# Kernel tuning notes

Hardware: AMD Instinct MI355X
Metric: run time of the kernel (lower is better)

The kernel has to match this reference:

```python
import jax, jax.numpy as jnp
import numpy as np

HIDDEN_NF = 256
ATOMICA_DIM = 512
NUM_HEADS = 4
HEAD_DIM = HIDDEN_NF // NUM_HEADS
EDGE_CUTOFF = 10.0
N_LIG = 1024
N_POCKET = 8192
BOX = 30.0  # Angstrom box so the cutoff mask is selective


def _lin(key, fan_in, fan_out):
    kw, kb = jax.random.split(key)
    s = 1.0 / np.sqrt(fan_in)
    W = jax.random.uniform(kw, (fan_in, fan_out), jnp.float32, -s, s)
    b = jax.random.uniform(kb, (fan_out,), jnp.float32, -s, s)
    return W, b


def setup_inputs() -> dict:
    key = jax.random.key(0)
    ks = jax.random.split(key, 12)
    h_lig = jax.random.normal(ks[0], (N_LIG, HIDDEN_NF), jnp.float32)
    x_lig = jax.random.uniform(ks[1], (N_LIG, 3), jnp.float32) * BOX
    h_atomica = jax.random.normal(ks[2], (N_POCKET, ATOMICA_DIM), jnp.float32)
    x_pocket = jax.random.uniform(ks[3], (N_POCKET, 3), jnp.float32) * BOX
    qw, qb = _lin(ks[4], HIDDEN_NF, HIDDEN_NF)
    kw, kb = _lin(ks[5], ATOMICA_DIM, HIDDEN_NF)
    vw, vb = _lin(ks[6], ATOMICA_DIM, HIDDEN_NF)
    ow, ob = _lin(ks[7], HIDDEN_NF, HIDDEN_NF)
    e1w, e1b = _lin(ks[8], 1, HIDDEN_NF)
    e2w, e2b = _lin(ks[9], HIDDEN_NF, NUM_HEADS)
    c1w, c1b = _lin(ks[10], HIDDEN_NF, HIDDEN_NF)
    c2w, c2b = _lin(ks[11], HIDDEN_NF, 1)
    return dict(h_lig=h_lig, x_lig=x_lig, h_atomica=h_atomica, x_pocket=x_pocket,
                qw=qw, qb=qb, kw=kw, kb=kb, vw=vw, vb=vb, ow=ow, ob=ob,
                e1w=e1w, e1b=e1b, e2w=e2w, e2b=e2b,
                c1w=c1w, c1b=c1b, c2w=c2w, c2b=c2b)


def reference(h_lig, x_lig, h_atomica, x_pocket,
              qw, qb, kw, kb, vw, vb, ow, ob,
              e1w, e1b, e2w, e2b, c1w, c1b, c2w, c2b):
    N_lig = h_lig.shape[0]
    silu = jax.nn.silu
    # pairwise geometry: [N_lig, N_pocket, 3]
    rel_pos = x_pocket[None, :, :] - x_lig[:, None, :]
    distances = jnp.linalg.norm(rel_pos, axis=-1, keepdims=True)  # [Nl,Np,1]
    # edge bias MLP: [Nl,Np,num_heads]
    edge_attr = silu(distances @ e1w + e1b) @ e2w + e2b
    mask = distances[..., 0] < EDGE_CUTOFF  # [Nl,Np]
    Q = (h_lig @ qw + qb).reshape(N_lig, NUM_HEADS, HEAD_DIM)
    K = (h_atomica @ kw + kb).reshape(-1, NUM_HEADS, HEAD_DIM)
    V = (h_atomica @ vw + vb).reshape(-1, NUM_HEADS, HEAD_DIM)
    scores = jnp.einsum('ihd,jhd->ijh', Q, K) / np.sqrt(HEAD_DIM).astype(np.float32)
    scores = scores + edge_attr
    scores = jnp.where(mask[..., None], scores, -jnp.inf)
    attn = jax.nn.softmax(scores, axis=1)
    attn = jnp.where(jnp.isnan(attn), 0.0, attn)  # nan_to_num for fully-masked rows
    h_attended = jnp.einsum('ijh,jhd->ihd', attn, V).reshape(N_lig, HIDDEN_NF)
    h_out = h_lig + h_attended @ ow + ob
    # equivariant coordinate update
    normalized_rel_pos = rel_pos / (distances + 1e-8)
    avg_attn = attn.mean(axis=-1, keepdims=True)  # [Nl,Np,1]
    coord_messages = (avg_attn * normalized_rel_pos).sum(axis=1)  # [Nl,3]
    coord_scale = silu(h_attended @ c1w + c1b) @ c2w + c2b  # [Nl,1]
    x_out = x_lig + coord_scale * coord_messages
    return h_out, x_out
```

## Files before the change

kernel.cpp:

```cpp
#include <hip/hip_runtime.h>
#include <hip/hip_bf16.h>


#define NLIG   1024
#define NPOCK  8192
#define HIDDEN 256
#define ADIM   512
#define NHEAD  4
#define HDIM   64
#define NTAB   1024
#define NSPLIT 32
#define CHUNK  (NPOCK / NSPLIT)
#define LOG2E  1.4426950408889634f
#define QK_SCALE (0.125f * LOG2E)

typedef float f32x16 __attribute__((ext_vector_type(16)));
typedef short short8 __attribute__((ext_vector_type(8)));

union U4S8 { uint4 u; short8 s; };

static __device__ __forceinline__ float exp2h(float x) {
  float r; asm("v_exp_f32 %0, %1" : "=v"(r) : "v"(x)); return r;
}
static __device__ __forceinline__ float rsqh(float x) {
  float r; asm("v_rsq_f32 %0, %1" : "=v"(r) : "v"(x)); return r;
}
static __device__ __forceinline__ unsigned cvtpk(float lo, float hi) {
  unsigned r;
  asm("v_cvt_pk_bf16_f32 %0, %1, %2" : "=v"(r) : "v"(lo), "v"(hi));
  return r;
}
static __device__ __forceinline__ unsigned short f2bf(float f) {
  union { __hip_bfloat16 h; unsigned short u; } c;
  c.h = __float2bfloat16(f);
  return c.u;
}
static __device__ __forceinline__ float bf2f(unsigned u16) {
  union { unsigned uu; float f; } c;
  c.uu = u16 << 16;
  return c.f;
}
static __device__ __forceinline__ short8 load_bf8(const unsigned short* p) {
  U4S8 t; t.u = *(const uint4*)p; return t.s;
}
static __device__ __forceinline__ f32x16 mfma32(short8 a, short8 b, f32x16 c) {
  return __builtin_amdgcn_mfma_f32_32x32x16_bf16(a, b, c, 0, 0, 0);
}

#define NCAST 4352
#define NTRANS 448
__global__ __launch_bounds__(256)
void prep_kernel(const float* __restrict__ hA, const float* __restrict__ hl,
                 const float* __restrict__ qw, const float* __restrict__ kw,
                 const float* __restrict__ vw, const float* __restrict__ ow,
                 const float* __restrict__ c1w,
                 const float* __restrict__ e1w, const float* __restrict__ e1b,
                 const float* __restrict__ e2w, const float* __restrict__ e2b,
                 unsigned short* __restrict__ hAb, unsigned short* __restrict__ hlb,
                 unsigned short* __restrict__ qwT, unsigned short* __restrict__ kwT,
                 unsigned short* __restrict__ vwT, unsigned short* __restrict__ owT,
                 unsigned short* __restrict__ c1wT, float* __restrict__ tabG) {
  int bx = blockIdx.x;
  int tid = threadIdx.x;
  if (bx < NCAST) {
    int id = bx * 256 + tid;
    const int nA4 = NPOCK * ADIM / 4;
    if (id < nA4) {
      float4 v = ((const float4*)hA)[id];
      ushort4 o; o.x = f2bf(v.x); o.y = f2bf(v.y); o.z = f2bf(v.z); o.w = f2bf(v.w);
      ((ushort4*)hAb)[id] = o;
    } else {
      int j = id - nA4;
      float4 v = ((const float4*)hl)[j];
      ushort4 o; o.x = f2bf(v.x); o.y = f2bf(v.y); o.z = f2bf(v.z); o.w = f2bf(v.w);
      ((ushort4*)hlb)[j] = o;
    }
  } else if (bx < NCAST + NTRANS) {
    int b = bx - NCAST;
    const float* src; unsigned short* dst; int K;
    if (b < 64)       { src = qw;  dst = qwT;  K = 256; }
    else if (b < 192) { src = kw;  dst = kwT;  K = 512; b -= 64; }
    else if (b < 320) { src = vw;  dst = vwT;  K = 512; b -= 192; }
    else if (b < 384) { src = ow;  dst = owT;  K = 256; b -= 320; }
    else              { src = c1w; dst = c1wT; K = 256; b -= 384; }
    int kt = K / 32;
    int k0 = (b % kt) * 32, n0 = (b / kt) * 32;
    __shared__ float tile[32][33];
    int tx = tid & 31, ty = tid >> 5;
#pragma unroll
    for (int r = 0; r < 4; ++r)
      tile[ty + 8 * r][tx] = src[(k0 + ty + 8 * r) * 256 + n0 + tx];
    __syncthreads();
#pragma unroll
    for (int r = 0; r < 4; ++r)
      dst[(n0 + ty + 8 * r) * K + k0 + tx] = f2bf(tile[tx][ty + 8 * r]);
  } else {
    int eb = bx - (NCAST + NTRANS);
    int w = tid >> 6, l = tid & 63;
    int entry = eb * 4 + w;
    float d = (entry + 0.5f) * (10.0f / NTAB);
    float a0 = 0.f, a1 = 0.f, a2 = 0.f, a3 = 0.f;
#pragma unroll
    for (int jj = 0; jj < 4; ++jj) {
      int j = l + jj * 64;
      float v = fmaf(d, e1w[j], e1b[j]);
      float s = v / (1.0f + __expf(-v));
      float4 w2 = ((const float4*)e2w)[j];
      a0 = fmaf(s, w2.x, a0);
      a1 = fmaf(s, w2.y, a1);
      a2 = fmaf(s, w2.z, a2);
      a3 = fmaf(s, w2.w, a3);
    }
#pragma unroll
    for (int m = 32; m >= 1; m >>= 1) {
      a0 += __shfl_xor(a0, m); a1 += __shfl_xor(a1, m);
      a2 += __shfl_xor(a2, m); a3 += __shfl_xor(a3, m);
    }
    if (l == 0) {
      tabG[0 * NTAB + entry] = (a0 + e2b[0]) * LOG2E;
      tabG[1 * NTAB + entry] = (a1 + e2b[1]) * LOG2E;
      tabG[2 * NTAB + entry] = (a2 + e2b[2]) * LOG2E;
      tabG[3 * NTAB + entry] = (a3 + e2b[3]) * LOG2E;
    }
  }
}

__global__ __launch_bounds__(256)
void kv_gemm_kernel(const unsigned short* __restrict__ hAb,
                    const unsigned short* __restrict__ kwT, const unsigned short* __restrict__ vwT,
                    const float* __restrict__ kb, const float* __restrict__ vb,
                    unsigned short* __restrict__ Kb, unsigned short* __restrict__ VTb) {
  int tid = threadIdx.x;
  int w = tid >> 6, lane = tid & 63;
  int lo = lane & 31, hi = lane >> 5;
  int m0 = blockIdx.x * 128 + w * 32;
  int n0 = blockIdx.y * 32;
  const unsigned short* ap  = hAb + (size_t)(m0 + lo) * ADIM + hi * 8;
  const unsigned short* bkp = kwT + (size_t)(n0 + lo) * ADIM + hi * 8;
  const unsigned short* bvp = vwT + (size_t)(n0 + lo) * ADIM + hi * 8;
  f32x16 aK, aV;
#pragma unroll
  for (int i = 0; i < 16; ++i) { aK[i] = 0.f; aV[i] = 0.f; }
#pragma unroll 8
  for (int kk = 0; kk < ADIM / 16; ++kk) {
    short8 a  = load_bf8(ap + kk * 16);
    short8 bk = load_bf8(bkp + kk * 16);
    short8 bv = load_bf8(bvp + kk * 16);
    aK = mfma32(a, bk, aK);
    aV = mfma32(bv, a, aV);
  }
  int n = n0 + lo;
  float bnK = kb[n];
#pragma unroll
  for (int g = 0; g < 4; ++g) {
#pragma unroll
    for (int rr = 0; rr < 4; ++rr) {
      int r = g * 4 + rr;
      int row = g * 8 + hi * 4 + rr;
      Kb[(size_t)(m0 + row) * HIDDEN + n] = f2bf(aK[r] + bnK);
      int nv = n0 + row;
      VTb[(size_t)nv * NPOCK + m0 + lo] = f2bf(aV[r] + vb[nv]);
    }
  }
}

template <int MODE>
__global__ __launch_bounds__(64)
void gemm32_kernel(const unsigned short* __restrict__ A, const unsigned short* __restrict__ BT,
                   const float* __restrict__ bias, void* __restrict__ out,
                   const float* __restrict__ resid, int M, int N, int K) {
  int lane = threadIdx.x;
  int lo = lane & 31, hi = lane >> 5;
  int m0 = blockIdx.x * 32, n0 = blockIdx.y * 32;
  const unsigned short* ap = A + (size_t)(m0 + lo) * K + hi * 8;
  const unsigned short* bp = BT + (size_t)(n0 + lo) * K + hi * 8;
  f32x16 acc;
#pragma unroll
  for (int i = 0; i < 16; ++i) acc[i] = 0.f;
  int nk = K / 16;
#pragma unroll 4
  for (int kk = 0; kk < nk; ++kk) {
    short8 a = load_bf8(ap + kk * 16);
    short8 b = load_bf8(bp + kk * 16);
    acc = mfma32(a, b, acc);
  }
  int n = n0 + lo;
  float bn = bias[n];
#pragma unroll
  for (int g = 0; g < 4; ++g) {
#pragma unroll
    for (int rr = 0; rr < 4; ++rr) {
      int r = g * 4 + rr;
      int m = m0 + g * 8 + hi * 4 + rr;
      float v = acc[r] + bn;
      if (MODE == 0) {
        ((unsigned short*)out)[(size_t)m * N + n] = f2bf(v);
      } else if (MODE == 2) {
        ((float*)out)[(size_t)m * N + n] = v + resid[(size_t)m * N + n];
      } else {
        float sg = v / (1.0f + exp2h(-LOG2E * v));
        ((unsigned short*)out)[(size_t)m * N + n] = f2bf(sg);
      }
    }
  }
}

__global__ __launch_bounds__(256)
void attn_kernel(const unsigned short* __restrict__ Qbf, const unsigned short* __restrict__ Kbf,
                 const unsigned short* __restrict__ VTbf,
                 const float* __restrict__ x_lig, const float* __restrict__ x_pocket,
                 const float* __restrict__ tabG,
                 unsigned* __restrict__ partOb, float4* __restrict__ partZC) {
  __shared__ float4 xch[CHUNK];
  __shared__ float tab[NHEAD][NTAB];

  int tid = threadIdx.x;
  int h = tid >> 6;
  int lane = tid & 63;
  int lo = lane & 31, hi = lane >> 5;
  int qt = blockIdx.x & 31;
  int split = blockIdx.x >> 5;
  int q0 = qt * 32;
  int j0g = split * CHUNK;

  for (int i = tid; i < CHUNK; i += 256) {
    float x = x_pocket[(j0g + i) * 3 + 0];
    float y = x_pocket[(j0g + i) * 3 + 1];
    float z = x_pocket[(j0g + i) * 3 + 2];
    float4 v; v.x = x; v.y = y; v.z = z; v.w = 0.f;
    xch[i] = v;
  }
  for (int i = tid; i < NHEAD * NTAB; i += 256) ((float*)tab)[i] = tabG[i];
  __syncthreads();

  int q = q0 + lo;
  float xl0 = x_lig[q * 3 + 0];
  float xl1 = x_lig[q * 3 + 1];
  float xl2 = x_lig[q * 3 + 2];

  short8 qfr[4];
#pragma unroll
  for (int kk = 0; kk < 4; ++kk)
    qfr[kk] = load_bf8(Qbf + (size_t)q * HIDDEN + h * HDIM + kk * 16 + hi * 8);

  f32x16 O0, O1;
#pragma unroll
  for (int i = 0; i < 16; ++i) { O0[i] = 0.f; O1[i] = 0.f; }
  float Z = 0.f, c0 = 0.f, c1 = 0.f, c2 = 0.f;

#pragma unroll 1
  for (int t = 0; t < CHUNK / 32; ++t) {
    int jb = t * 32;
    f32x16 s;
#pragma unroll
    for (int i = 0; i < 16; ++i) s[i] = 0.f;
#pragma unroll
    for (int kk = 0; kk < 4; ++kk) {
      short8 a = load_bf8(Kbf + (size_t)(j0g + jb + lo) * HIDDEN + h * HDIM + kk * 16 + hi * 8);
      s = mfma32(a, qfr[kk], s);
    }
    unsigned wp[8];
    float pprev = 0.f;
#pragma unroll
    for (int r = 0; r < 16; ++r) {
      int jl = (r & 3) + 8 * (r >> 2) + 4 * hi;
      float4 xp = xch[jb + jl];
      float dx = xp.x - xl0, dy = xp.y - xl1, dz = xp.z - xl2;
      float r2 = fmaf(dx, dx, fmaf(dy, dy, dz * dz));
      float r2c = fmaxf(r2, 1e-24f);
      float rinv = rsqh(r2c);
      float d = r2c * rinv;
      int idx = (int)(d * (NTAB / 10.0f));
      idx = idx > (NTAB - 1) ? (NTAB - 1) : idx;
      float b = tab[h][idx];
      float s2 = fmaf(s[r], QK_SCALE, b);
      float pe = (r2 < 100.0f) ? exp2h(s2) : 0.0f;
      Z += pe;
      float pr = pe * rinv;
      c0 = fmaf(pr, dx, c0);
      c1 = fmaf(pr, dy, c1);
      c2 = fmaf(pr, dz, c2);
      if (r & 1) wp[r >> 1] = cvtpk(pprev, pe); else pprev = pe;
    }
#pragma unroll
    for (int sub = 0; sub < 2; ++sub) {
      unsigned W0 = wp[sub * 4 + 0], W1 = wp[sub * 4 + 1];
      unsigned W2 = wp[sub * 4 + 2], W3 = wp[sub * 4 + 3];
      unsigned e01 = (unsigned)__shfl_xor((int)(hi ? W0 : W2), 32);
      unsigned e23 = (unsigned)__shfl_xor((int)(hi ? W1 : W3), 32);
      U4S8 pb;
      pb.u.x = hi ? e01 : W0;
      pb.u.y = hi ? e23 : W1;
      pb.u.z = hi ? W2 : e01;
      pb.u.w = hi ? W3 : e23;
      const unsigned short* vbase =
          VTbf + (size_t)(h * HDIM + lo) * NPOCK + j0g + jb + sub * 16 + hi * 8;
      short8 v0 = load_bf8(vbase);
      short8 v1 = load_bf8(vbase + (size_t)32 * NPOCK);
      O0 = mfma32(v0, pb.s, O0);
      O1 = mfma32(v1, pb.s, O1);
    }
  }

  unsigned* po = partOb + (size_t)(((q * NHEAD) + h) * NSPLIT + split) * (HDIM / 2);
#pragma unroll
  for (int g = 0; g < 4; ++g) {
    uint2 u0;
    u0.x = cvtpk(O0[g * 4 + 0], O0[g * 4 + 1]);
    u0.y = cvtpk(O0[g * 4 + 2], O0[g * 4 + 3]);
    *(uint2*)(po + (g * 8 + hi * 4) / 2) = u0;
    uint2 u1;
    u1.x = cvtpk(O1[g * 4 + 0], O1[g * 4 + 1]);
    u1.y = cvtpk(O1[g * 4 + 2], O1[g * 4 + 3]);
    *(uint2*)(po + (32 + g * 8 + hi * 4) / 2) = u1;
  }
  float Zt = Z + __shfl_xor(Z, 32);
  float c0t = c0 + __shfl_xor(c0, 32);
  float c1t = c1 + __shfl_xor(c1, 32);
  float c2t = c2 + __shfl_xor(c2, 32);
  if (hi == 0) {
    float4 zc; zc.x = Zt; zc.y = c0t; zc.z = c1t; zc.w = c2t;
    partZC[((q * NHEAD) + h) * NSPLIT + split] = zc;
  }
}

__global__ __launch_bounds__(256)
void combine_kernel(const unsigned short* __restrict__ partOb, const float4* __restrict__ partZC,
                    unsigned short* __restrict__ hattb, float* __restrict__ cmsg) {
  int q = blockIdx.x;
  int t = threadIdx.x;
  int h = t >> 6, dl = t & 63;
  float Zh = 0.f;
#pragma unroll
  for (int s = 0; s < NSPLIT; ++s) Zh += partZC[(q * NHEAD + h) * NSPLIT + s].x;
  float o = 0.f;
#pragma unroll
  for (int s = 0; s < NSPLIT; ++s)
    o += bf2f(partOb[(size_t)((q * NHEAD + h) * NSPLIT + s) * HDIM + dl]);
  float inv = (Zh > 0.f) ? 1.0f / Zh : 0.f;
  hattb[(size_t)q * HIDDEN + h * HDIM + dl] = f2bf(o * inv);

  __shared__ float sm[NHEAD][3];
  if (t < NHEAD) {
    float zz = 0.f, a0 = 0.f, a1 = 0.f, a2 = 0.f;
    for (int s = 0; s < NSPLIT; ++s) {
      float4 v = partZC[(q * NHEAD + t) * NSPLIT + s];
      zz += v.x; a0 += v.y; a1 += v.z; a2 += v.w;
    }
    float iv = (zz > 0.f) ? 0.25f / zz : 0.f;
    sm[t][0] = a0 * iv; sm[t][1] = a1 * iv; sm[t][2] = a2 * iv;
  }
  __syncthreads();
  if (t < 3) cmsg[q * 3 + t] = sm[0][t] + sm[1][t] + sm[2][t] + sm[3][t];
}

__global__ __launch_bounds__(64)
void coord_kernel(const unsigned short* __restrict__ c1out, const float* __restrict__ c2w,
                  const float* __restrict__ c2b, const float* __restrict__ cmsg,
                  const float* __restrict__ x_lig, float* __restrict__ x_out) {
  int q = blockIdx.x;
  int lane = threadIdx.x;
  const unsigned short* row = c1out + (size_t)q * HIDDEN + lane * 4;
  ushort4 tv = *(const ushort4*)row;
  float4 wv = *(const float4*)(c2w + lane * 4);
  float acc = bf2f(tv.x) * wv.x + bf2f(tv.y) * wv.y + bf2f(tv.z) * wv.z + bf2f(tv.w) * wv.w;
#pragma unroll
  for (int m = 32; m >= 1; m >>= 1) acc += __shfl_xor(acc, m);
  if (lane == 0) {
    float sc = acc + c2b[0];
    x_out[q * 3 + 0] = x_lig[q * 3 + 0] + sc * cmsg[q * 3 + 0];
    x_out[q * 3 + 1] = x_lig[q * 3 + 1] + sc * cmsg[q * 3 + 1];
    x_out[q * 3 + 2] = x_lig[q * 3 + 2] + sc * cmsg[q * 3 + 2];
  }
}

extern "C" void kernel_launch(void* const* d_in, const int* in_sizes, int n_in,
                              void* d_out, int out_size, void* d_ws, size_t ws_size,
                              hipStream_t stream) {
  const float* h_lig  = (const float*)d_in[0];
  const float* x_lig  = (const float*)d_in[1];
  const float* h_atom = (const float*)d_in[2];
  const float* x_pock = (const float*)d_in[3];
  const float* qw  = (const float*)d_in[4];
  const float* qb  = (const float*)d_in[5];
  const float* kw  = (const float*)d_in[6];
  const float* kb  = (const float*)d_in[7];
  const float* vw  = (const float*)d_in[8];
  const float* vb  = (const float*)d_in[9];
  const float* ow  = (const float*)d_in[10];
  const float* ob  = (const float*)d_in[11];
  const float* e1w = (const float*)d_in[12];
  const float* e1b = (const float*)d_in[13];
  const float* e2w = (const float*)d_in[14];
  const float* e2b = (const float*)d_in[15];
  const float* c1w = (const float*)d_in[16];
  const float* c1b = (const float*)d_in[17];
  const float* c2w = (const float*)d_in[18];
  const float* c2b = (const float*)d_in[19];

  char* w = (char*)d_ws;
  unsigned short* hAb  = (unsigned short*)w; w += (size_t)NPOCK * ADIM * 2;
  unsigned short* hlb  = (unsigned short*)w; w += (size_t)NLIG * HIDDEN * 2;
  unsigned short* qwT  = (unsigned short*)w; w += 256 * 256 * 2;
  unsigned short* kwT  = (unsigned short*)w; w += 256 * 512 * 2;
  unsigned short* vwT  = (unsigned short*)w; w += 256 * 512 * 2;
  unsigned short* owT  = (unsigned short*)w; w += 256 * 256 * 2;
  unsigned short* c1wT = (unsigned short*)w; w += 256 * 256 * 2;
  unsigned short* Qb   = (unsigned short*)w; w += (size_t)NLIG * HIDDEN * 2;
  unsigned short* Kb   = (unsigned short*)w; w += (size_t)NPOCK * HIDDEN * 2;
  unsigned short* VTb  = (unsigned short*)w; w += (size_t)HIDDEN * NPOCK * 2;
  float* tabG          = (float*)w;          w += NHEAD * NTAB * 4;
  unsigned* partOb     = (unsigned*)w;       w += (size_t)NLIG * NHEAD * NSPLIT * HDIM * 2;
  float* partZC        = (float*)w;          w += (size_t)NLIG * NHEAD * NSPLIT * 4 * 4;
  unsigned short* hatt = (unsigned short*)w; w += (size_t)NLIG * HIDDEN * 2;
  unsigned short* c1o  = (unsigned short*)w; w += (size_t)NLIG * HIDDEN * 2;
  float* cmsg          = (float*)w;          w += (size_t)NLIG * 3 * 4;

  float* hout = (float*)d_out;
  float* xout = ((float*)d_out) + (size_t)NLIG * HIDDEN;

  prep_kernel<<<NCAST + NTRANS + NTAB / 4, 256, 0, stream>>>(
      h_atom, h_lig, qw, kw, vw, ow, c1w, e1w, e1b, e2w, e2b,
      hAb, hlb, qwT, kwT, vwT, owT, c1wT, tabG);
  kv_gemm_kernel<<<dim3(NPOCK / 128, HIDDEN / 32), 256, 0, stream>>>(
      hAb, kwT, vwT, kb, vb, Kb, VTb);
  gemm32_kernel<0><<<dim3(NLIG / 32, HIDDEN / 32), 64, 0, stream>>>(
      hlb, qwT, qb, (void*)Qb, nullptr, NLIG, HIDDEN, HIDDEN);
  attn_kernel<<<32 * NSPLIT, 256, 0, stream>>>(Qb, Kb, VTb, x_lig, x_pock, tabG,
                                               partOb, (float4*)partZC);
  combine_kernel<<<NLIG, 256, 0, stream>>>((const unsigned short*)partOb,
                                           (const float4*)partZC, hatt, cmsg);
  gemm32_kernel<2><<<dim3(NLIG / 32, HIDDEN / 32), 64, 0, stream>>>(
      hatt, owT, ob, (void*)hout, h_lig, NLIG, HIDDEN, HIDDEN);
  gemm32_kernel<3><<<dim3(NLIG / 32, HIDDEN / 32), 64, 0, stream>>>(
      hatt, c1wT, c1b, (void*)c1o, nullptr, NLIG, HIDDEN, HIDDEN);
  coord_kernel<<<NLIG, 64, 0, stream>>>(c1o, c2w, c2b, cmsg, x_lig, xout);
}
```

Before: 208.7 us.

## Fuse Q/KV projections and output epilogue GEMMs, prefetch K/V in attention, halve splits

Merges the Q projection into the K/V projection kernel and merges the output projection, the coord MLP GEMM and the c2 dot product into one epilogue kernel that uses atomics to accumulate the coordinate scale. The attention loop now prefetches the next K tile and the current V tiles before the MFMAs to hide load latency, and the sequence split count drops from 32 to 16. The aim is fewer launches and better latency hiding, at the cost of less attention-grid parallelism, an extra memset, and atomic accumulation order that makes the coordinate scale nondeterministic.

```diff
diff --git a/kernel.cpp b/kernel.cpp
--- a/kernel.cpp
+++ b/kernel.cpp
@@ -9,8 +9,9 @@
 #define NHEAD  4
 #define HDIM   64
 #define NTAB   1024
-#define NSPLIT 32
+#define NSPLIT 16
 #define CHUNK  (NPOCK / NSPLIT)
+#define NT     (CHUNK / 32)
 #define LOG2E  1.4426950408889634f
 #define QK_SCALE (0.125f * LOG2E)
 
@@ -126,80 +127,67 @@
 }
 
 __global__ __launch_bounds__(256)
-void kv_gemm_kernel(const unsigned short* __restrict__ hAb,
-                    const unsigned short* __restrict__ kwT, const unsigned short* __restrict__ vwT,
-                    const float* __restrict__ kb, const float* __restrict__ vb,
-                    unsigned short* __restrict__ Kb, unsigned short* __restrict__ VTb) {
+void proj_kernel(const unsigned short* __restrict__ hAb, const unsigned short* __restrict__ hlb,
+                 const unsigned short* __restrict__ kwT, const unsigned short* __restrict__ vwT,
+                 const unsigned short* __restrict__ qwT,
+                 const float* __restrict__ kb, const float* __restrict__ vb,
+                 const float* __restrict__ qb,
+                 unsigned short* __restrict__ Kb, unsigned short* __restrict__ VTb,
+                 unsigned short* __restrict__ Qb) {
   int tid = threadIdx.x;
   int w = tid >> 6, lane = tid & 63;
   int lo = lane & 31, hi = lane >> 5;
-  int m0 = blockIdx.x * 128 + w * 32;
   int n0 = blockIdx.y * 32;
-  const unsigned short* ap  = hAb + (size_t)(m0 + lo) * ADIM + hi * 8;
-  const unsigned short* bkp = kwT + (size_t)(n0 + lo) * ADIM + hi * 8;
-  const unsigned short* bvp = vwT + (size_t)(n0 + lo) * ADIM + hi * 8;
-  f32x16 aK, aV;
-#pragma unroll
-  for (int i = 0; i < 16; ++i) { aK[i] = 0.f; aV[i] = 0.f; }
+  int n = n0 + lo;
+  if (blockIdx.x < 64) {
+    int m0 = blockIdx.x * 128 + w * 32;
+    const unsigned short* ap  = hAb + (size_t)(m0 + lo) * ADIM + hi * 8;
+    const unsigned short* bkp = kwT + (size_t)n * ADIM + hi * 8;
+    const unsigned short* bvp = vwT + (size_t)n * ADIM + hi * 8;
+    f32x16 aK, aV;
+#pragma unroll
+    for (int i = 0; i < 16; ++i) { aK[i] = 0.f; aV[i] = 0.f; }
 #pragma unroll 8
-  for (int kk = 0; kk < ADIM / 16; ++kk) {
-    short8 a  = load_bf8(ap + kk * 16);
-    short8 bk = load_bf8(bkp + kk * 16);
-    short8 bv = load_bf8(bvp + kk * 16);
-    aK = mfma32(a, bk, aK);
-    aV = mfma32(bv, a, aV);
-  }
-  int n = n0 + lo;
-  float bnK = kb[n];
-#pragma unroll
-  for (int g = 0; g < 4; ++g) {
-#pragma unroll
-    for (int rr = 0; rr < 4; ++rr) {
-      int r = g * 4 + rr;
-      int row = g * 8 + hi * 4 + rr;
-      Kb[(size_t)(m0 + row) * HIDDEN + n] = f2bf(aK[r] + bnK);
-      int nv = n0 + row;
-      VTb[(size_t)nv * NPOCK + m0 + lo] = f2bf(aV[r] + vb[nv]);
-    }
-  }
-}
-
-template <int MODE>
-__global__ __launch_bounds__(64)
-void gemm32_kernel(const unsigned short* __restrict__ A, const unsigned short* __restrict__ BT,
-                   const float* __restrict__ bias, void* __restrict__ out,
-                   const float* __restrict__ resid, int M, int N, int K) {
-  int lane = threadIdx.x;
-  int lo = lane & 31, hi = lane >> 5;
-  int m0 = blockIdx.x * 32, n0 = blockIdx.y * 32;
-  const unsigned short* ap = A + (size_t)(m0 + lo) * K + hi * 8;
-  const unsigned short* bp = BT + (size_t)(n0 + lo) * K + hi * 8;
-  f32x16 acc;
-#pragma unroll
-  for (int i = 0; i < 16; ++i) acc[i] = 0.f;
-  int nk = K / 16;
-#pragma unroll 4
-  for (int kk = 0; kk < nk; ++kk) {
-    short8 a = load_bf8(ap + kk * 16);
-    short8 b = load_bf8(bp + kk * 16);
-    acc = mfma32(a, b, acc);
-  }
-  int n = n0 + lo;
-  float bn = bias[n];
-#pragma unroll
-  for (int g = 0; g < 4; ++g) {
-#pragma unroll
-    for (int rr = 0; rr < 4; ++rr) {
-      int r = g * 4 + rr;
-      int m = m0 + g * 8 + hi * 4 + rr;
-      float v = acc[r] + bn;
-      if (MODE == 0) {
-        ((unsigned short*)out)[(size_t)m * N + n] = f2bf(v);
-      } else if (MODE == 2) {
-        ((float*)out)[(size_t)m * N + n] = v + resid[(size_t)m * N + n];
-      } else {
-        float sg = v / (1.0f + exp2h(-LOG2E * v));
-        ((unsigned short*)out)[(size_t)m * N + n] = f2bf(sg);
+    for (int kk = 0; kk < ADIM / 16; ++kk) {
+      short8 a  = load_bf8(ap + kk * 16);
+      short8 bk = load_bf8(bkp + kk * 16);
+      short8 bv = load_bf8(bvp + kk * 16);
+      aK = mfma32(a, bk, aK);
+      aV = mfma32(bv, a, aV);
+    }
+    float bnK = kb[n];
+#pragma unroll
+    for (int g = 0; g < 4; ++g) {
+#pragma unroll
+      for (int rr = 0; rr < 4; ++rr) {
+        int r = g * 4 + rr;
+        int row = g * 8 + hi * 4 + rr;
+        Kb[(size_t)(m0 + row) * HIDDEN + n] = f2bf(aK[r] + bnK);
+        int nv = n0 + row;
+        VTb[(size_t)nv * NPOCK + m0 + lo] = f2bf(aV[r] + vb[nv]);
+      }
+    }
+  } else {
+    int m0 = (blockIdx.x - 64) * 128 + w * 32;
+    const unsigned short* ap = hlb + (size_t)(m0 + lo) * HIDDEN + hi * 8;
+    const unsigned short* bp = qwT + (size_t)n * HIDDEN + hi * 8;
+    f32x16 acc;
+#pragma unroll
+    for (int i = 0; i < 16; ++i) acc[i] = 0.f;
+#pragma unroll 8
+    for (int kk = 0; kk < HIDDEN / 16; ++kk) {
+      short8 a = load_bf8(ap + kk * 16);
+      short8 b = load_bf8(bp + kk * 16);
+      acc = mfma32(a, b, acc);
+    }
+    float bn = qb[n];
+#pragma unroll
+    for (int g = 0; g < 4; ++g) {
+#pragma unroll
+      for (int rr = 0; rr < 4; ++rr) {
+        int r = g * 4 + rr;
+        int m = m0 + g * 8 + hi * 4 + rr;
+        Qb[(size_t)m * HIDDEN + n] = f2bf(acc[r] + bn);
       }
     }
   }
@@ -243,22 +231,39 @@
   for (int kk = 0; kk < 4; ++kk)
     qfr[kk] = load_bf8(Qbf + (size_t)q * HIDDEN + h * HDIM + kk * 16 + hi * 8);
 
+  const unsigned short* kbp = Kbf + (size_t)(j0g + lo) * HIDDEN + h * HDIM + hi * 8;
+  const unsigned short* vbp = VTbf + (size_t)(h * HDIM + lo) * NPOCK + j0g + hi * 8;
+
   f32x16 O0, O1;
 #pragma unroll
   for (int i = 0; i < 16; ++i) { O0[i] = 0.f; O1[i] = 0.f; }
   float Z = 0.f, c0 = 0.f, c1 = 0.f, c2 = 0.f;
 
+  short8 kcur[4];
+#pragma unroll
+  for (int kk = 0; kk < 4; ++kk) kcur[kk] = load_bf8(kbp + kk * 16);
+
 #pragma unroll 1
-  for (int t = 0; t < CHUNK / 32; ++t) {
+  for (int t = 0; t < NT; ++t) {
     int jb = t * 32;
+    int tn = (t + 1 < NT) ? (t + 1) : t;
+    short8 knx0 = load_bf8(kbp + (size_t)tn * 32 * HIDDEN + 0 * 16);
+    short8 knx1 = load_bf8(kbp + (size_t)tn * 32 * HIDDEN + 1 * 16);
+    short8 knx2 = load_bf8(kbp + (size_t)tn * 32 * HIDDEN + 2 * 16);
+    short8 knx3 = load_bf8(kbp + (size_t)tn * 32 * HIDDEN + 3 * 16);
+    short8 v00 = load_bf8(vbp + jb);
+    short8 v01 = load_bf8(vbp + jb + (size_t)32 * NPOCK);
+    short8 v10 = load_bf8(vbp + jb + 16);
+    short8 v11 = load_bf8(vbp + jb + 16 + (size_t)32 * NPOCK);
+
     f32x16 s;
 #pragma unroll
     for (int i = 0; i < 16; ++i) s[i] = 0.f;
-#pragma unroll
-    for (int kk = 0; kk < 4; ++kk) {
-      short8 a = load_bf8(Kbf + (size_t)(j0g + jb + lo) * HIDDEN + h * HDIM + kk * 16 + hi * 8);
-      s = mfma32(a, qfr[kk], s);
-    }
+    s = mfma32(kcur[0], qfr[0], s);
+    s = mfma32(kcur[1], qfr[1], s);
+    s = mfma32(kcur[2], qfr[2], s);
+    s = mfma32(kcur[3], qfr[3], s);
+
     unsigned wp[8];
     float pprev = 0.f;
 #pragma unroll
@@ -282,10 +287,8 @@
       c2 = fmaf(pr, dz, c2);
       if (r & 1) wp[r >> 1] = cvtpk(pprev, pe); else pprev = pe;
     }
-#pragma unroll
-    for (int sub = 0; sub < 2; ++sub) {
-      unsigned W0 = wp[sub * 4 + 0], W1 = wp[sub * 4 + 1];
-      unsigned W2 = wp[sub * 4 + 2], W3 = wp[sub * 4 + 3];
+    {
+      unsigned W0 = wp[0], W1 = wp[1], W2 = wp[2], W3 = wp[3];
       unsigned e01 = (unsigned)__shfl_xor((int)(hi ? W0 : W2), 32);
       unsigned e23 = (unsigned)__shfl_xor((int)(hi ? W1 : W3), 32);
       U4S8 pb;
@@ -293,13 +296,22 @@
       pb.u.y = hi ? e23 : W1;
       pb.u.z = hi ? W2 : e01;
       pb.u.w = hi ? W3 : e23;
-      const unsigned short* vbase =
-          VTbf + (size_t)(h * HDIM + lo) * NPOCK + j0g + jb + sub * 16 + hi * 8;
-      short8 v0 = load_bf8(vbase);
-      short8 v1 = load_bf8(vbase + (size_t)32 * NPOCK);
-      O0 = mfma32(v0, pb.s, O0);
-      O1 = mfma32(v1, pb.s, O1);
-    }
+      O0 = mfma32(v00, pb.s, O0);
+      O1 = mfma32(v01, pb.s, O1);
+    }
+    {
+      unsigned W0 = wp[4], W1 = wp[5], W2 = wp[6], W3 = wp[7];
+      unsigned e01 = (unsigned)__shfl_xor((int)(hi ? W0 : W2), 32);
+      unsigned e23 = (unsigned)__shfl_xor((int)(hi ? W1 : W3), 32);
+      U4S8 pb;
+      pb.u.x = hi ? e01 : W0;
+      pb.u.y = hi ? e23 : W1;
+      pb.u.z = hi ? W2 : e01;
+      pb.u.w = hi ? W3 : e23;
+      O0 = mfma32(v10, pb.s, O0);
+      O1 = mfma32(v11, pb.s, O1);
+    }
+    kcur[0] = knx0; kcur[1] = knx1; kcur[2] = knx2; kcur[3] = knx3;
   }
 
   unsigned* po = partOb + (size_t)(((q * NHEAD) + h) * NSPLIT + split) * (HDIM / 2);
@@ -354,23 +366,58 @@
   if (t < 3) cmsg[q * 3 + t] = sm[0][t] + sm[1][t] + sm[2][t] + sm[3][t];
 }
 
-__global__ __launch_bounds__(64)
-void coord_kernel(const unsigned short* __restrict__ c1out, const float* __restrict__ c2w,
-                  const float* __restrict__ c2b, const float* __restrict__ cmsg,
-                  const float* __restrict__ x_lig, float* __restrict__ x_out) {
-  int q = blockIdx.x;
-  int lane = threadIdx.x;
-  const unsigned short* row = c1out + (size_t)q * HIDDEN + lane * 4;
-  ushort4 tv = *(const ushort4*)row;
-  float4 wv = *(const float4*)(c2w + lane * 4);
-  float acc = bf2f(tv.x) * wv.x + bf2f(tv.y) * wv.y + bf2f(tv.z) * wv.z + bf2f(tv.w) * wv.w;
-#pragma unroll
-  for (int m = 32; m >= 1; m >>= 1) acc += __shfl_xor(acc, m);
-  if (lane == 0) {
-    float sc = acc + c2b[0];
-    x_out[q * 3 + 0] = x_lig[q * 3 + 0] + sc * cmsg[q * 3 + 0];
-    x_out[q * 3 + 1] = x_lig[q * 3 + 1] + sc * cmsg[q * 3 + 1];
-    x_out[q * 3 + 2] = x_lig[q * 3 + 2] + sc * cmsg[q * 3 + 2];
+__global__ __launch_bounds__(256)
+void epi_kernel(const unsigned short* __restrict__ hatt,
+                const unsigned short* __restrict__ owT, const unsigned short* __restrict__ c1wT,
+                const float* __restrict__ ob, const float* __restrict__ c1b,
+                const float* __restrict__ c2w, const float* __restrict__ h_lig,
+                float* __restrict__ hout, float* __restrict__ cscale) {
+  int tid = threadIdx.x;
+  int w = tid >> 6, lane = tid & 63;
+  int lo = lane & 31, hi = lane >> 5;
+  int m0 = blockIdx.x * 128 + w * 32;
+  int n0 = blockIdx.y * 32;
+  int n = n0 + lo;
+  const unsigned short* ap = hatt + (size_t)(m0 + lo) * HIDDEN + hi * 8;
+  const unsigned short* bo = owT + (size_t)n * HIDDEN + hi * 8;
+  const unsigned short* bc = c1wT + (size_t)n * HIDDEN + hi * 8;
+  f32x16 aO, aC;
+#pragma unroll
+  for (int i = 0; i < 16; ++i) { aO[i] = 0.f; aC[i] = 0.f; }
+#pragma unroll 8
+  for (int kk = 0; kk < HIDDEN / 16; ++kk) {
+    short8 a  = load_bf8(ap + kk * 16);
+    short8 b1 = load_bf8(bo + kk * 16);
+    short8 b2 = load_bf8(bc + kk * 16);
+    aO = mfma32(a, b1, aO);
+    aC = mfma32(a, b2, aC);
+  }
+  float obn = ob[n], c1bn = c1b[n], c2wn = c2w[n];
+#pragma unroll
+  for (int g = 0; g < 4; ++g) {
+#pragma unroll
+    for (int rr = 0; rr < 4; ++rr) {
+      int r = g * 4 + rr;
+      int m = m0 + g * 8 + hi * 4 + rr;
+      hout[(size_t)m * HIDDEN + n] = aO[r] + obn + h_lig[(size_t)m * HIDDEN + n];
+      float v = aC[r] + c1bn;
+      float sg = v / (1.0f + exp2h(-LOG2E * v));
+      float part = sg * c2wn;
+#pragma unroll
+      for (int msk = 16; msk >= 1; msk >>= 1) part += __shfl_xor(part, msk);
+      if (lo == 0) atomicAdd(&cscale[m], part);
+    }
+  }
+}
+
+__global__ __launch_bounds__(256)
+void coordfin_kernel(const float* __restrict__ cscale, const float* __restrict__ c2b,
+                     const float* __restrict__ cmsg, const float* __restrict__ x_lig,
+                     float* __restrict__ x_out) {
+  int id = blockIdx.x * 256 + threadIdx.x;
+  if (id < NLIG * 3) {
+    int q = id / 3;
+    x_out[id] = x_lig[id] + (cscale[q] + c2b[0]) * cmsg[id];
   }
 }
 
@@ -413,8 +460,8 @@
   unsigned* partOb     = (unsigned*)w;       w += (size_t)NLIG * NHEAD * NSPLIT * HDIM * 2;
   float* partZC        = (float*)w;          w += (size_t)NLIG * NHEAD * NSPLIT * 4 * 4;
   unsigned short* hatt = (unsigned short*)w; w += (size_t)NLIG * HIDDEN * 2;
-  unsigned short* c1o  = (unsigned short*)w; w += (size_t)NLIG * HIDDEN * 2;
   float* cmsg          = (float*)w;          w += (size_t)NLIG * 3 * 4;
+  float* cscale        = (float*)w;          w += (size_t)NLIG * 4;
 
   float* hout = (float*)d_out;
   float* xout = ((float*)d_out) + (size_t)NLIG * HIDDEN;
@@ -422,17 +469,15 @@
   prep_kernel<<<NCAST + NTRANS + NTAB / 4, 256, 0, stream>>>(
       h_atom, h_lig, qw, kw, vw, ow, c1w, e1w, e1b, e2w, e2b,
       hAb, hlb, qwT, kwT, vwT, owT, c1wT, tabG);
-  kv_gemm_kernel<<<dim3(NPOCK / 128, HIDDEN / 32), 256, 0, stream>>>(
-      hAb, kwT, vwT, kb, vb, Kb, VTb);
-  gemm32_kernel<0><<<dim3(NLIG / 32, HIDDEN / 32), 64, 0, stream>>>(
-      hlb, qwT, qb, (void*)Qb, nullptr, NLIG, HIDDEN, HIDDEN);
+  proj_kernel<<<dim3(72, 8), 256, 0, stream>>>(
+      hAb, hlb, kwT, vwT, qwT, kb, vb, qb, Kb, VTb, Qb);
   attn_kernel<<<32 * NSPLIT, 256, 0, stream>>>(Qb, Kb, VTb, x_lig, x_pock, tabG,
                                                partOb, (float4*)partZC);
   combine_kernel<<<NLIG, 256, 0, stream>>>((const unsigned short*)partOb,
                                            (const float4*)partZC, hatt, cmsg);
-  gemm32_kernel<2><<<dim3(NLIG / 32, HIDDEN / 32), 64, 0, stream>>>(
-      hatt, owT, ob, (void*)hout, h_lig, NLIG, HIDDEN, HIDDEN);
-  gemm32_kernel<3><<<dim3(NLIG / 32, HIDDEN / 32), 64, 0, stream>>>(
-      hatt, c1wT, c1b, (void*)c1o, nullptr, NLIG, HIDDEN, HIDDEN);
-  coord_kernel<<<NLIG, 64, 0, stream>>>(c1o, c2w, c2b, cmsg, x_lig, xout);
-}
+  hipMemsetAsync(cscale, 0, NLIG * sizeof(float), stream);
+  epi_kernel<<<dim3(8, 8), 256, 0, stream>>>(hatt, owT, c1wT, ob, c1b, c2w, h_lig,
+                                             hout, cscale);
+  coordfin_kernel<<<(NLIG * 3 + 255) / 256, 256, 0, stream>>>(cscale, c2b, cmsg,
+                                                              x_lig, xout);
+}
```

Result: no change. 208.7 us (+0.0%).
